# Optimization experiments

Measured on AMD Instinct MI355X. Metric: run time of the kernel, lower is better.

The kernel has to match this reference:

```python
import jax, jax.numpy as jnp
import numpy as np
import math

B, T, D, H = 2, 2048, 1024, 16
HD = D // H
FF = 4 * D
EPS = 1e-5


def rmsnorm(x, w):
    norm = jax.lax.rsqrt(jnp.mean(x * x, axis=-1, keepdims=True) + EPS)
    return x * norm * w


def setup_inputs() -> dict:
    key = jax.random.key(0)
    ks = jax.random.split(key, 10)
    s = 0.02
    x = jax.random.normal(ks[0], (B, T, D), dtype=jnp.float32)
    causal_mask = jnp.tril(jnp.ones((1, T, T), dtype=jnp.int32))
    # weights stored (in, out) so y = x @ W (equivalent to torch Linear with W.T)
    Wq = jax.random.normal(ks[1], (D, D), dtype=jnp.float32) * s
    Wk = jax.random.normal(ks[2], (D, D), dtype=jnp.float32) * s
    Wv = jax.random.normal(ks[3], (D, D), dtype=jnp.float32) * s
    Wo = jax.random.normal(ks[4], (D, D), dtype=jnp.float32) * s
    bo = jnp.zeros((D,), dtype=jnp.float32)
    W1 = jax.random.normal(ks[5], (D, FF), dtype=jnp.float32) * s
    b1 = jnp.zeros((FF,), dtype=jnp.float32)
    W2 = jax.random.normal(ks[6], (FF, D), dtype=jnp.float32) * s
    b2 = jnp.zeros((D,), dtype=jnp.float32)
    g_attn = jnp.ones((D,), dtype=jnp.float32)
    g_ff = jnp.ones((D,), dtype=jnp.float32)
    return dict(x=x, causal_mask=causal_mask, Wq=Wq, Wk=Wk, Wv=Wv, Wo=Wo, bo=bo,
                W1=W1, b1=b1, W2=W2, b2=b2, g_attn=g_attn, g_ff=g_ff)


def reference(x, causal_mask, Wq, Wk, Wv, Wo, bo, W1, b1, W2, b2, g_attn, g_ff):
    b, t, d = x.shape
    xa = rmsnorm(x, g_attn)
    # project and split heads: (b, h, t, hd)
    q = (xa @ Wq).reshape(b, t, H, HD).transpose(0, 2, 1, 3)
    k = (xa @ Wk).reshape(b, t, H, HD).transpose(0, 2, 1, 3)
    v = (xa @ Wv).reshape(b, t, H, HD).transpose(0, 2, 1, 3)
    scores = jnp.einsum('bhqd,bhkd->bhqk', q, k) / math.sqrt(HD)
    mask = causal_mask[:, None, :t, :t]  # (1,1,t,t)
    scores = jnp.where(mask == 0, jnp.float32(-1e9), scores)
    probs = jax.nn.softmax(scores, axis=-1)
    attn = jnp.einsum('bhqk,bhkd->bhqd', probs, v)
    attn = attn.transpose(0, 2, 1, 3).reshape(b, t, d)
    x = x + attn @ Wo + bo
    xf = rmsnorm(x, g_ff)
    h = jax.nn.silu(xf @ W1 + b1)
    x = x + h @ W2 + b2
    return x
```

## Files before the change

### kernel.cpp

```cpp
#include <hip/hip_runtime.h>
#include <hip/hip_bf16.h>
#include <cstdint>
#include <cstddef>

#define Bn 2
#define Tn 2048
#define Dn 1024
#define Hn 16
#define HDn 64
#define FFn 4096
#define Mrows (Bn*Tn)

typedef __bf16 bf16x8 __attribute__((ext_vector_type(8)));
typedef float  f32x4  __attribute__((ext_vector_type(4)));

__device__ __forceinline__ unsigned short f2bf(float f) {
  unsigned int u = __float_as_uint(f);
  unsigned int r = (u + 0x7FFFu + ((u >> 16) & 1u)) >> 16;
  return (unsigned short)r;
}

__device__ __forceinline__ void gload_lds16(const unsigned short* g, unsigned short* l) {
  __builtin_amdgcn_global_load_lds(
      (const __attribute__((address_space(1))) unsigned int*)g,
      (__attribute__((address_space(3))) unsigned int*)l, 16, 0, 0);
}

__device__ __forceinline__ f32x4 mfma16(bf16x8 a, bf16x8 b, f32x4 c) {
  return __builtin_amdgcn_mfma_f32_16x16x32_bf16(a, b, c, 0, 0, 0);
}

__global__ void cast_transpose(const float* __restrict__ in, unsigned short* __restrict__ out,
                               int R, int C) {
  __shared__ float tile[32][33];
  int c0 = blockIdx.x * 32, r0 = blockIdx.y * 32;
  int x = threadIdx.x, y = threadIdx.y;
  #pragma unroll
  for (int i = 0; i < 32; i += 8)
    tile[y + i][x] = in[(size_t)(r0 + y + i) * C + c0 + x];
  __syncthreads();
  #pragma unroll
  for (int i = 0; i < 32; i += 8)
    out[(size_t)(c0 + y + i) * R + r0 + x] = f2bf(tile[x][y + i]);
}

__global__ __launch_bounds__(256) void rmsnorm_cast(const float* __restrict__ x,
                                                    const float* __restrict__ g,
                                                    unsigned short* __restrict__ out) {
  __shared__ float ssum[4];
  int row = blockIdx.x;
  int tid = threadIdx.x;
  const float4* xr = (const float4*)(x + (size_t)row * Dn);
  float4 v = xr[tid];
  float ss = v.x * v.x + v.y * v.y + v.z * v.z + v.w * v.w;
  #pragma unroll
  for (int m = 32; m; m >>= 1) ss += __shfl_xor(ss, m);
  if ((tid & 63) == 0) ssum[tid >> 6] = ss;
  __syncthreads();
  float tot = ssum[0] + ssum[1] + ssum[2] + ssum[3];
  float nrm = rsqrtf(tot * (1.0f / Dn) + 1e-5f);
  float4 gv = ((const float4*)g)[tid];
  ushort4 o;
  o.x = f2bf(v.x * nrm * gv.x);
  o.y = f2bf(v.y * nrm * gv.y);
  o.z = f2bf(v.z * nrm * gv.z);
  o.w = f2bf(v.w * nrm * gv.w);
  ((ushort4*)out)[(size_t)row * (Dn / 4) + tid] = o;
}

#define BM 128
#define BN 128
#define BK 64
template <int EPI>
__global__ __launch_bounds__(256, 2) void gemm_bt(
    const unsigned short* __restrict__ A, const unsigned short* __restrict__ Bt,
    unsigned short* __restrict__ outB, float* __restrict__ outF,
    const float* __restrict__ bias, const float* __restrict__ resid,
    int Mdim, int Ndim, int Kdim) {
  __shared__ __align__(16) unsigned short As[BM * BK];
  __shared__ __align__(16) unsigned short Bs[BN * BK];
  const int tid = threadIdx.x;
  const int lane = tid & 63, w = tid >> 6;
  const int wr = w >> 1, wc = w & 1;
  const int lr = lane & 15, lg = lane >> 4;
  const int m0 = blockIdx.y * BM, n0 = blockIdx.x * BN;

  f32x4 acc[4][4] = {};
  const int kiters = Kdim / BK;
  for (int kt = 0; kt < kiters; ++kt) {
    const int k0 = kt * BK;
    #pragma unroll
    for (int i = 0; i < 4; ++i) {
      int c = tid + i * 256;
      int row = c >> 3, sl = c & 7, g = sl ^ (row & 7);
      gload_lds16(A + (size_t)(m0 + row) * Kdim + k0 + g * 8, &As[c * 8]);
    }
    #pragma unroll
    for (int i = 0; i < 4; ++i) {
      int c = tid + i * 256;
      int row = c >> 3, sl = c & 7, g = sl ^ (row & 7);
      gload_lds16(Bt + (size_t)(n0 + row) * Kdim + k0 + g * 8, &Bs[c * 8]);
    }
    asm volatile("s_waitcnt vmcnt(0)");
    __syncthreads();
    #pragma unroll
    for (int kk = 0; kk < 2; ++kk) {
      bf16x8 af[4], bfr[4];
      #pragma unroll
      for (int mi = 0; mi < 4; ++mi) {
        int row = wr * 64 + mi * 16 + lr;
        int sl = (kk * 4 + lg) ^ (row & 7);
        af[mi] = *(const bf16x8*)&As[row * BK + sl * 8];
      }
      #pragma unroll
      for (int ni = 0; ni < 4; ++ni) {
        int row = wc * 64 + ni * 16 + lr;
        int sl = (kk * 4 + lg) ^ (row & 7);
        bfr[ni] = *(const bf16x8*)&Bs[row * BK + sl * 8];
      }
      #pragma unroll
      for (int mi = 0; mi < 4; ++mi)
        #pragma unroll
        for (int ni = 0; ni < 4; ++ni)
          acc[mi][ni] = mfma16(af[mi], bfr[ni], acc[mi][ni]);
    }
    __syncthreads();
  }
  #pragma unroll
  for (int mi = 0; mi < 4; ++mi) {
    #pragma unroll
    for (int ni = 0; ni < 4; ++ni) {
      #pragma unroll
      for (int rg = 0; rg < 4; ++rg) {
        int r = m0 + wr * 64 + mi * 16 + lg * 4 + rg;
        int c = n0 + wc * 64 + ni * 16 + lr;
        float v = acc[mi][ni][rg];
        if (EPI == 0) {
          outB[(size_t)r * Ndim + c] = f2bf(v);
        } else if (EPI == 1) {
          int b = r >> 11, t = r & (Tn - 1);
          int hh = c >> 6, hd = c & 63;
          outB[(((size_t)((b * Hn + hh) * HDn + hd)) << 11) + t] = f2bf(v);
        } else if (EPI == 2) {
          outF[(size_t)r * Ndim + c] = v + bias[c] + resid[(size_t)r * Ndim + c];
        } else {
          float vb = v + bias[c];
          float s = vb / (1.0f + __expf(-vb));
          outB[(size_t)r * Ndim + c] = f2bf(s);
        }
      }
    }
  }
}

__global__ __launch_bounds__(256, 2) void attn_fwd(
    const unsigned short* __restrict__ Q, const unsigned short* __restrict__ Kb,
    const unsigned short* __restrict__ Vt, unsigned short* __restrict__ O) {
  __shared__ __align__(16) unsigned short Ks[64 * 64];
  __shared__ __align__(16) unsigned short Vs[64 * 64];
  __shared__ __align__(16) unsigned short Ps[4][16 * 64];
  const int tid = threadIdx.x, lane = tid & 63, w = tid >> 6;
  const int lr = lane & 15, lg = lane >> 4;
  const int bh = blockIdx.y, b = bh >> 4, h = bh & 15;
  const int qb = blockIdx.x * 64;
  const int qw = qb + w * 16;

  const size_t qrow = ((size_t)(b * Tn) + qw + lr) * Dn + h * HDn;
  bf16x8 qf0 = *(const bf16x8*)&Q[qrow + lg * 8];
  bf16x8 qf1 = *(const bf16x8*)&Q[qrow + 32 + lg * 8];

  f32x4 ao[4] = {};
  float mrow[4], lsum[4];
  #pragma unroll
  for (int rg = 0; rg < 4; ++rg) { mrow[rg] = -1e30f; lsum[rg] = 0.f; }

  const int nkt = blockIdx.x + 1;
  for (int kb = 0; kb < nkt; ++kb) {
    #pragma unroll
    for (int i = 0; i < 2; ++i) {
      int c = tid + i * 256;
      int row = c >> 3, sl = c & 7, g = sl ^ (row & 7);
      gload_lds16(Kb + ((size_t)(b * Tn) + kb * 64 + row) * Dn + h * HDn + g * 8, &Ks[c * 8]);
    }
    #pragma unroll
    for (int i = 0; i < 2; ++i) {
      int c = tid + i * 256;
      int row = c >> 3, sl = c & 7, g = sl ^ (row & 7);
      gload_lds16(Vt + (((size_t)((b * Hn + h) * HDn + row)) << 11) + kb * 64 + g * 8, &Vs[c * 8]);
    }
    asm volatile("s_waitcnt vmcnt(0)");
    __syncthreads();

    float p[4][4];
    #pragma unroll
    for (int sub = 0; sub < 4; ++sub) {
      f32x4 s = {};
      int row = sub * 16 + lr;
      bf16x8 k0 = *(const bf16x8*)&Ks[row * 64 + ((0 + lg) ^ (row & 7)) * 8];
      bf16x8 k1 = *(const bf16x8*)&Ks[row * 64 + ((4 + lg) ^ (row & 7)) * 8];
      s = mfma16(qf0, k0, s);
      s = mfma16(qf1, k1, s);
      #pragma unroll
      for (int rg = 0; rg < 4; ++rg) {
        int qg = qw + lg * 4 + rg;
        int kg = kb * 64 + sub * 16 + lr;
        p[sub][rg] = (kg > qg) ? -1e30f : s[rg] * 0.125f;
      }
    }
    #pragma unroll
    for (int rg = 0; rg < 4; ++rg) {
      float mt = fmaxf(fmaxf(p[0][rg], p[1][rg]), fmaxf(p[2][rg], p[3][rg]));
      #pragma unroll
      for (int msk = 1; msk < 16; msk <<= 1) mt = fmaxf(mt, __shfl_xor(mt, msk));
      float mnew = fmaxf(mrow[rg], mt);
      float sc = __expf(mrow[rg] - mnew);
      float rs = 0.f;
      #pragma unroll
      for (int sub = 0; sub < 4; ++sub) {
        p[sub][rg] = __expf(p[sub][rg] - mnew);
        rs += p[sub][rg];
      }
      #pragma unroll
      for (int msk = 1; msk < 16; msk <<= 1) rs += __shfl_xor(rs, msk);
      lsum[rg] = lsum[rg] * sc + rs;
      mrow[rg] = mnew;
      #pragma unroll
      for (int n = 0; n < 4; ++n) ao[n][rg] *= sc;
    }
    #pragma unroll
    for (int sub = 0; sub < 4; ++sub)
      #pragma unroll
      for (int rg = 0; rg < 4; ++rg) {
        int row = lg * 4 + rg;
        int col = sub * 16 + lr;
        int sl = (col >> 3) ^ (row & 7);
        Ps[w][row * 64 + sl * 8 + (col & 7)] = f2bf(p[sub][rg]);
      }
    bf16x8 pf0 = *(const bf16x8*)&Ps[w][lr * 64 + ((0 + lg) ^ (lr & 7)) * 8];
    bf16x8 pf1 = *(const bf16x8*)&Ps[w][lr * 64 + ((4 + lg) ^ (lr & 7)) * 8];
    #pragma unroll
    for (int n = 0; n < 4; ++n) {
      int vrow = n * 16 + lr;
      bf16x8 v0 = *(const bf16x8*)&Vs[vrow * 64 + ((0 + lg) ^ (vrow & 7)) * 8];
      bf16x8 v1 = *(const bf16x8*)&Vs[vrow * 64 + ((4 + lg) ^ (vrow & 7)) * 8];
      ao[n] = mfma16(pf0, v0, ao[n]);
      ao[n] = mfma16(pf1, v1, ao[n]);
    }
    __syncthreads();
  }
  #pragma unroll
  for (int rg = 0; rg < 4; ++rg) {
    float inv = 1.0f / lsum[rg];
    int r = b * Tn + qw + lg * 4 + rg;
    #pragma unroll
    for (int n = 0; n < 4; ++n)
      O[(size_t)r * Dn + h * HDn + n * 16 + lr] = f2bf(ao[n][rg] * inv);
  }
}

extern "C" void kernel_launch(void* const* d_in, const int* in_sizes, int n_in,
                              void* d_out, int out_size, void* d_ws, size_t ws_size,
                              hipStream_t stream) {
  const float* x      = (const float*)d_in[0];
  const float* Wq     = (const float*)d_in[2];
  const float* Wk     = (const float*)d_in[3];
  const float* Wv     = (const float*)d_in[4];
  const float* Wo     = (const float*)d_in[5];
  const float* bo     = (const float*)d_in[6];
  const float* W1     = (const float*)d_in[7];
  const float* b1     = (const float*)d_in[8];
  const float* W2     = (const float*)d_in[9];
  const float* b2     = (const float*)d_in[10];
  const float* g_attn = (const float*)d_in[11];
  const float* g_ff   = (const float*)d_in[12];
  float* out = (float*)d_out;

  char* ws = (char*)d_ws;
  size_t off = 0;
  auto carve = [&](size_t bytes) {
    void* p = ws + off;
    off += (bytes + 255) & ~(size_t)255;
    return p;
  };
  const size_t MD2 = (size_t)Mrows * Dn * 2;
  unsigned short* xa   = (unsigned short*)carve(MD2);
  unsigned short* qb   = (unsigned short*)carve(MD2);
  unsigned short* kb   = (unsigned short*)carve(MD2);
  unsigned short* vt   = (unsigned short*)carve(MD2);
  float*          xmid = (float*)carve((size_t)Mrows * Dn * 4);
  unsigned short* hbuf = (unsigned short*)carve((size_t)Mrows * FFn * 2);
  unsigned short* Wqt  = (unsigned short*)carve((size_t)Dn * Dn * 2);
  unsigned short* Wkt  = (unsigned short*)carve((size_t)Dn * Dn * 2);
  unsigned short* Wvt  = (unsigned short*)carve((size_t)Dn * Dn * 2);
  unsigned short* Wot  = (unsigned short*)carve((size_t)Dn * Dn * 2);
  unsigned short* W1t  = (unsigned short*)carve((size_t)Dn * FFn * 2);
  unsigned short* W2t  = (unsigned short*)carve((size_t)Dn * FFn * 2);

  dim3 tb(32, 8);
  cast_transpose<<<dim3(Dn / 32, Dn / 32), tb, 0, stream>>>(Wq, Wqt, Dn, Dn);
  cast_transpose<<<dim3(Dn / 32, Dn / 32), tb, 0, stream>>>(Wk, Wkt, Dn, Dn);
  cast_transpose<<<dim3(Dn / 32, Dn / 32), tb, 0, stream>>>(Wv, Wvt, Dn, Dn);
  cast_transpose<<<dim3(Dn / 32, Dn / 32), tb, 0, stream>>>(Wo, Wot, Dn, Dn);
  cast_transpose<<<dim3(FFn / 32, Dn / 32), tb, 0, stream>>>(W1, W1t, Dn, FFn);
  cast_transpose<<<dim3(Dn / 32, FFn / 32), tb, 0, stream>>>(W2, W2t, FFn, Dn);

  rmsnorm_cast<<<Mrows, 256, 0, stream>>>(x, g_attn, xa);

  gemm_bt<0><<<dim3(Dn / BN, Mrows / BM), 256, 0, stream>>>(xa, Wqt, qb, nullptr, nullptr, nullptr, Mrows, Dn, Dn);
  gemm_bt<0><<<dim3(Dn / BN, Mrows / BM), 256, 0, stream>>>(xa, Wkt, kb, nullptr, nullptr, nullptr, Mrows, Dn, Dn);
  gemm_bt<1><<<dim3(Dn / BN, Mrows / BM), 256, 0, stream>>>(xa, Wvt, vt, nullptr, nullptr, nullptr, Mrows, Dn, Dn);

  attn_fwd<<<dim3(Tn / 64, Bn * Hn), 256, 0, stream>>>(qb, kb, vt, xa);

  gemm_bt<2><<<dim3(Dn / BN, Mrows / BM), 256, 0, stream>>>(xa, Wot, nullptr, xmid, bo, x, Mrows, Dn, Dn);

  rmsnorm_cast<<<Mrows, 256, 0, stream>>>(xmid, g_ff, qb);

  gemm_bt<3><<<dim3(FFn / BN, Mrows / BM), 256, 0, stream>>>(qb, W1t, hbuf, nullptr, b1, nullptr, Mrows, FFn, Dn);
  gemm_bt<2><<<dim3(Dn / BN, Mrows / BM), 256, 0, stream>>>(hbuf, W2t, nullptr, out, b2, xmid, Mrows, Dn, FFn);
}
```

Measured before the change: 470.8 us.

## Fuse QKV projections into one GEMM and double-buffer attention K/V tiles

The three Q/K/V projection GEMMs become one GEMM over a concatenated transposed weight, with an epilogue that routes each column range to the q, k or transposed-v buffer. The attention kernel now double-buffers its K/V shared-memory tiles so the next tile's global-to-LDS load is issued while the current tile is computed. It also uses exp2 with a log2e-prescaled softmax scale, a 1-D grid that permutes causal query blocks to even out per-block work, and a higher occupancy target in launch bounds. The explicit vmcnt wait before using a prefetched tile was removed, so correctness relies on the barrier covering the async LDS loads. The extra LDS buffers may also limit the higher occupancy target.

```diff
diff --git a/kernel.cpp b/kernel.cpp
--- a/kernel.cpp
+++ b/kernel.cpp
@@ -74,7 +74,8 @@
 template <int EPI>
 __global__ __launch_bounds__(256, 2) void gemm_bt(
     const unsigned short* __restrict__ A, const unsigned short* __restrict__ Bt,
-    unsigned short* __restrict__ outB, float* __restrict__ outF,
+    unsigned short* __restrict__ outB, unsigned short* __restrict__ outB2,
+    unsigned short* __restrict__ outB3, float* __restrict__ outF,
     const float* __restrict__ bias, const float* __restrict__ resid,
     int Mdim, int Ndim, int Kdim) {
   __shared__ __align__(16) unsigned short As[BM * BK];
@@ -143,26 +144,39 @@
           outB[(((size_t)((b * Hn + hh) * HDn + hd)) << 11) + t] = f2bf(v);
         } else if (EPI == 2) {
           outF[(size_t)r * Ndim + c] = v + bias[c] + resid[(size_t)r * Ndim + c];
-        } else {
+        } else if (EPI == 3) {
           float vb = v + bias[c];
           float s = vb / (1.0f + __expf(-vb));
           outB[(size_t)r * Ndim + c] = f2bf(s);
+        } else {
+          if (n0 < Dn) {
+            outB[(size_t)r * Dn + c] = f2bf(v);
+          } else if (n0 < 2 * Dn) {
+            outB2[(size_t)r * Dn + (c - Dn)] = f2bf(v);
+          } else {
+            int b = r >> 11, t = r & (Tn - 1);
+            int cc = c - 2 * Dn;
+            int hh = cc >> 6, hd = cc & 63;
+            outB3[(((size_t)((b * Hn + hh) * HDn + hd)) << 11) + t] = f2bf(v);
+          }
         }
       }
     }
   }
 }
 
-__global__ __launch_bounds__(256, 2) void attn_fwd(
+__global__ __launch_bounds__(256, 4) void attn_fwd(
     const unsigned short* __restrict__ Q, const unsigned short* __restrict__ Kb,
     const unsigned short* __restrict__ Vt, unsigned short* __restrict__ O) {
-  __shared__ __align__(16) unsigned short Ks[64 * 64];
-  __shared__ __align__(16) unsigned short Vs[64 * 64];
+  __shared__ __align__(16) unsigned short Ks[2][64 * 64];
+  __shared__ __align__(16) unsigned short Vs[2][64 * 64];
   __shared__ __align__(16) unsigned short Ps[4][16 * 64];
   const int tid = threadIdx.x, lane = tid & 63, w = tid >> 6;
   const int lr = lane & 15, lg = lane >> 4;
-  const int bh = blockIdx.y, b = bh >> 4, h = bh & 15;
-  const int qb = blockIdx.x * 64;
+  const int id = blockIdx.x;
+  const int bh = id >> 5, b = bh >> 4, h = bh & 15;
+  const int qx = ((id & 31) + ((id >> 8) << 3)) & 31;
+  const int qb = qx * 64;
   const int qw = qb + w * 16;
 
   const size_t qrow = ((size_t)(b * Tn) + qw + lr) * Dn + h * HDn;
@@ -174,37 +188,48 @@
   #pragma unroll
   for (int rg = 0; rg < 4; ++rg) { mrow[rg] = -1e30f; lsum[rg] = 0.f; }
 
-  const int nkt = blockIdx.x + 1;
-  for (int kb = 0; kb < nkt; ++kb) {
+  const int nkt = qx + 1;
+  const size_t kbase = (size_t)(b * Tn) * Dn + h * HDn;
+  const size_t vbase = ((size_t)((b * Hn + h) * HDn)) << 11;
+
+  auto stage = [&](int buf, int kt) {
     #pragma unroll
     for (int i = 0; i < 2; ++i) {
       int c = tid + i * 256;
       int row = c >> 3, sl = c & 7, g = sl ^ (row & 7);
-      gload_lds16(Kb + ((size_t)(b * Tn) + kb * 64 + row) * Dn + h * HDn + g * 8, &Ks[c * 8]);
+      gload_lds16(Kb + kbase + (size_t)(kt * 64 + row) * Dn + g * 8, &Ks[buf][c * 8]);
     }
     #pragma unroll
     for (int i = 0; i < 2; ++i) {
       int c = tid + i * 256;
       int row = c >> 3, sl = c & 7, g = sl ^ (row & 7);
-      gload_lds16(Vt + (((size_t)((b * Hn + h) * HDn + row)) << 11) + kb * 64 + g * 8, &Vs[c * 8]);
-    }
-    asm volatile("s_waitcnt vmcnt(0)");
-    __syncthreads();
+      gload_lds16(Vt + vbase + ((size_t)row << 11) + kt * 64 + g * 8, &Vs[buf][c * 8]);
+    }
+  };
+
+  stage(0, 0);
+  __syncthreads();
+
+  const float cl2 = 0.125f * 1.44269504f;
+
+  for (int kt = 0; kt < nkt; ++kt) {
+    const int cur = kt & 1;
+    if (kt + 1 < nkt) stage(cur ^ 1, kt + 1);
 
     float p[4][4];
     #pragma unroll
     for (int sub = 0; sub < 4; ++sub) {
       f32x4 s = {};
       int row = sub * 16 + lr;
-      bf16x8 k0 = *(const bf16x8*)&Ks[row * 64 + ((0 + lg) ^ (row & 7)) * 8];
-      bf16x8 k1 = *(const bf16x8*)&Ks[row * 64 + ((4 + lg) ^ (row & 7)) * 8];
+      bf16x8 k0 = *(const bf16x8*)&Ks[cur][row * 64 + ((0 + lg) ^ (row & 7)) * 8];
+      bf16x8 k1 = *(const bf16x8*)&Ks[cur][row * 64 + ((4 + lg) ^ (row & 7)) * 8];
       s = mfma16(qf0, k0, s);
       s = mfma16(qf1, k1, s);
       #pragma unroll
       for (int rg = 0; rg < 4; ++rg) {
         int qg = qw + lg * 4 + rg;
-        int kg = kb * 64 + sub * 16 + lr;
-        p[sub][rg] = (kg > qg) ? -1e30f : s[rg] * 0.125f;
+        int kg = kt * 64 + sub * 16 + lr;
+        p[sub][rg] = (kg > qg) ? -1e30f : s[rg] * cl2;
       }
     }
     #pragma unroll
@@ -213,11 +238,11 @@
       #pragma unroll
       for (int msk = 1; msk < 16; msk <<= 1) mt = fmaxf(mt, __shfl_xor(mt, msk));
       float mnew = fmaxf(mrow[rg], mt);
-      float sc = __expf(mrow[rg] - mnew);
+      float sc = exp2f(mrow[rg] - mnew);
       float rs = 0.f;
       #pragma unroll
       for (int sub = 0; sub < 4; ++sub) {
-        p[sub][rg] = __expf(p[sub][rg] - mnew);
+        p[sub][rg] = exp2f(p[sub][rg] - mnew);
         rs += p[sub][rg];
       }
       #pragma unroll
@@ -241,8 +266,8 @@
     #pragma unroll
     for (int n = 0; n < 4; ++n) {
       int vrow = n * 16 + lr;
-      bf16x8 v0 = *(const bf16x8*)&Vs[vrow * 64 + ((0 + lg) ^ (vrow & 7)) * 8];
-      bf16x8 v1 = *(const bf16x8*)&Vs[vrow * 64 + ((4 + lg) ^ (vrow & 7)) * 8];
+      bf16x8 v0 = *(const bf16x8*)&Vs[cur][vrow * 64 + ((0 + lg) ^ (vrow & 7)) * 8];
+      bf16x8 v1 = *(const bf16x8*)&Vs[cur][vrow * 64 + ((4 + lg) ^ (vrow & 7)) * 8];
       ao[n] = mfma16(pf0, v0, ao[n]);
       ao[n] = mfma16(pf1, v1, ao[n]);
     }
@@ -283,39 +308,39 @@
     return p;
   };
   const size_t MD2 = (size_t)Mrows * Dn * 2;
-  unsigned short* xa   = (unsigned short*)carve(MD2);
-  unsigned short* qb   = (unsigned short*)carve(MD2);
-  unsigned short* kb   = (unsigned short*)carve(MD2);
-  unsigned short* vt   = (unsigned short*)carve(MD2);
-  float*          xmid = (float*)carve((size_t)Mrows * Dn * 4);
-  unsigned short* hbuf = (unsigned short*)carve((size_t)Mrows * FFn * 2);
-  unsigned short* Wqt  = (unsigned short*)carve((size_t)Dn * Dn * 2);
-  unsigned short* Wkt  = (unsigned short*)carve((size_t)Dn * Dn * 2);
-  unsigned short* Wvt  = (unsigned short*)carve((size_t)Dn * Dn * 2);
-  unsigned short* Wot  = (unsigned short*)carve((size_t)Dn * Dn * 2);
-  unsigned short* W1t  = (unsigned short*)carve((size_t)Dn * FFn * 2);
-  unsigned short* W2t  = (unsigned short*)carve((size_t)Dn * FFn * 2);
+  unsigned short* xa    = (unsigned short*)carve(MD2);
+  unsigned short* qb    = (unsigned short*)carve(MD2);
+  unsigned short* kb    = (unsigned short*)carve(MD2);
+  unsigned short* vt    = (unsigned short*)carve(MD2);
+  float*          xmid  = (float*)carve((size_t)Mrows * Dn * 4);
+  unsigned short* hbuf  = (unsigned short*)carve((size_t)Mrows * FFn * 2);
+  unsigned short* Wqkvt = (unsigned short*)carve((size_t)3 * Dn * Dn * 2);
+  unsigned short* Wot   = (unsigned short*)carve((size_t)Dn * Dn * 2);
+  unsigned short* W1t   = (unsigned short*)carve((size_t)Dn * FFn * 2);
+  unsigned short* W2t   = (unsigned short*)carve((size_t)Dn * FFn * 2);
 
   dim3 tb(32, 8);
-  cast_transpose<<<dim3(Dn / 32, Dn / 32), tb, 0, stream>>>(Wq, Wqt, Dn, Dn);
-  cast_transpose<<<dim3(Dn / 32, Dn / 32), tb, 0, stream>>>(Wk, Wkt, Dn, Dn);
-  cast_transpose<<<dim3(Dn / 32, Dn / 32), tb, 0, stream>>>(Wv, Wvt, Dn, Dn);
+  cast_transpose<<<dim3(Dn / 32, Dn / 32), tb, 0, stream>>>(Wq, Wqkvt, Dn, Dn);
+  cast_transpose<<<dim3(Dn / 32, Dn / 32), tb, 0, stream>>>(Wk, Wqkvt + (size_t)Dn * Dn, Dn, Dn);
+  cast_transpose<<<dim3(Dn / 32, Dn / 32), tb, 0, stream>>>(Wv, Wqkvt + (size_t)2 * Dn * Dn, Dn, Dn);
   cast_transpose<<<dim3(Dn / 32, Dn / 32), tb, 0, stream>>>(Wo, Wot, Dn, Dn);
   cast_transpose<<<dim3(FFn / 32, Dn / 32), tb, 0, stream>>>(W1, W1t, Dn, FFn);
   cast_transpose<<<dim3(Dn / 32, FFn / 32), tb, 0, stream>>>(W2, W2t, FFn, Dn);
 
   rmsnorm_cast<<<Mrows, 256, 0, stream>>>(x, g_attn, xa);
 
-  gemm_bt<0><<<dim3(Dn / BN, Mrows / BM), 256, 0, stream>>>(xa, Wqt, qb, nullptr, nullptr, nullptr, Mrows, Dn, Dn);
-  gemm_bt<0><<<dim3(Dn / BN, Mrows / BM), 256, 0, stream>>>(xa, Wkt, kb, nullptr, nullptr, nullptr, Mrows, Dn, Dn);
-  gemm_bt<1><<<dim3(Dn / BN, Mrows / BM), 256, 0, stream>>>(xa, Wvt, vt, nullptr, nullptr, nullptr, Mrows, Dn, Dn);
-
-  attn_fwd<<<dim3(Tn / 64, Bn * Hn), 256, 0, stream>>>(qb, kb, vt, xa);
-
-  gemm_bt<2><<<dim3(Dn / BN, Mrows / BM), 256, 0, stream>>>(xa, Wot, nullptr, xmid, bo, x, Mrows, Dn, Dn);
+  gemm_bt<4><<<dim3(3 * Dn / BN, Mrows / BM), 256, 0, stream>>>(
+      xa, Wqkvt, qb, kb, vt, nullptr, nullptr, nullptr, Mrows, 3 * Dn, Dn);
+
+  attn_fwd<<<dim3(1024), 256, 0, stream>>>(qb, kb, vt, xa);
+
+  gemm_bt<2><<<dim3(Dn / BN, Mrows / BM), 256, 0, stream>>>(
+      xa, Wot, nullptr, nullptr, nullptr, xmid, bo, x, Mrows, Dn, Dn);
 
   rmsnorm_cast<<<Mrows, 256, 0, stream>>>(xmid, g_ff, qb);
 
-  gemm_bt<3><<<dim3(FFn / BN, Mrows / BM), 256, 0, stream>>>(qb, W1t, hbuf, nullptr, b1, nullptr, Mrows, FFn, Dn);
-  gemm_bt<2><<<dim3(Dn / BN, Mrows / BM), 256, 0, stream>>>(hbuf, W2t, nullptr, out, b2, xmid, Mrows, Dn, FFn);
-}
+  gemm_bt<3><<<dim3(FFn / BN, Mrows / BM), 256, 0, stream>>>(
+      qb, W1t, hbuf, nullptr, nullptr, nullptr, b1, nullptr, Mrows, FFn, Dn);
+  gemm_bt<2><<<dim3(Dn / BN, Mrows / BM), 256, 0, stream>>>(
+      hbuf, W2t, nullptr, nullptr, nullptr, out, b2, xmid, Mrows, Dn, FFn);
+}
```

After: 433.2 us. 8.0% less time.
